# Performance work log

Measured on AMD Instinct MI355X. Metric: run time of the kernel, lower is better.

## Reference

```python
import jax, jax.numpy as jnp
import numpy as np

P, N, F, H, D_HID = 3, 4096, 1024, 8, 8
EMBED = H * D_HID  # 64
ATT, C = 128, 16


def setup_inputs() -> dict:
    key = jax.random.key(0)
    ks = jax.random.split(key, 12)
    return {
        "inputs": jax.random.normal(ks[0], (P, N, F), jnp.float32),
        # bias_mat plays the role of an additive adjacency mask; random floats are fine for math checking
        "bias_mat": jax.random.normal(ks[1], (P, N, N), jnp.float32),
        "W": jax.random.normal(ks[2], (P, H, F, D_HID), jnp.float32) * 0.05,
        "a1_w": jax.random.normal(ks[3], (P, H, D_HID), jnp.float32) * 0.1,
        "a1_b": jax.random.normal(ks[4], (P, H), jnp.float32) * 0.1,
        "a2_w": jax.random.normal(ks[5], (P, H, D_HID), jnp.float32) * 0.1,
        "a2_b": jax.random.normal(ks[6], (P, H), jnp.float32) * 0.1,
        "h_bias": jnp.zeros((P, H, D_HID), jnp.float32),
        "Ws": jax.random.normal(ks[7], (EMBED, ATT), jnp.float32) * 0.1,
        "bs": jax.random.normal(ks[8], (ATT,), jnp.float32) * 0.1,
        "u": jax.random.normal(ks[9], (ATT,), jnp.float32) * 0.1,
        "Wc": jax.random.normal(ks[10], (EMBED, C), jnp.float32) * 0.05,
        "bc": jnp.zeros((C,), jnp.float32),
    }


def reference(inputs, bias_mat, W, a1_w, a1_b, a2_w, a2_b, h_bias, Ws, bs, u, Wc, bc):
    # inputs: [P,N,F], bias_mat: [P,N,N]
    embeds = []
    for p in range(inputs.shape[0]):  # small fixed loop over meta-paths
        seq = inputs[p]                                            # [N,F]
        fts = jnp.einsum('nf,hfd->hnd', seq, W[p])                 # shared projection, all heads
        f1 = jnp.einsum('hnd,hd->hn', fts, a1_w[p]) + a1_b[p][:, None]
        f2 = jnp.einsum('hnd,hd->hn', fts, a2_w[p]) + a2_b[p][:, None]
        logits = f1[:, :, None] + f2[:, None, :]                   # [H,N,N] additive attention
        coefs = jax.nn.softmax(jax.nn.leaky_relu(logits) + bias_mat[p][None], axis=-1)
        vals = jnp.einsum('hnm,hmd->hnd', coefs, fts) + h_bias[p][:, None, :]
        h = jax.nn.elu(vals)                                       # activation per head
        embeds.append(jnp.transpose(h, (1, 0, 2)).reshape(h.shape[1], -1))  # concat heads -> [N,H*d]
    multi = jnp.stack(embeds, axis=1)                              # [N,P,EMBED]
    # semantic (meta-path) attention
    v = jnp.tanh(multi @ Ws + bs)                                  # [N,P,ATT]
    alphas = jax.nn.softmax(v @ u, axis=-1)                        # [N,P]
    final = jnp.sum(multi * alphas[:, :, None], axis=1)            # [N,EMBED]
    # single final classifier head (mean over 1 head == identity)
    logits_out = final @ Wc + bc                                   # [N,C]
    return logits_out, final, alphas
```

## Files before the change

kernel.cpp:

```cpp
#include <hip/hip_runtime.h>

#define LOG2E 1.44269504088896f

typedef _Float16 f16;
typedef _Float16 f16x8 __attribute__((ext_vector_type(8)));
typedef float f32x4 __attribute__((ext_vector_type(4)));

#define NP 3
#define NN 4096
#define FF 1024
#define HH 8
#define DD 8
#define HD 64

#define OFF_F1S   0
#define OFF_F2S   393216
#define OFF_F2MAX 589824
#define OFF_FTST  590080
#define OFF_MULTI 2162944

#define OUT_FINAL 65536
#define OUT_ALPHA 327680

__global__ __launch_bounds__(256) void kA(const float* __restrict__ inp,
                                          const float* __restrict__ W,
                                          const float* __restrict__ a1w,
                                          const float* __restrict__ a1b,
                                          const float* __restrict__ a2w,
                                          const float* __restrict__ a2b,
                                          char* __restrict__ ws) {
    __shared__ float At[32 * 36];
    __shared__ float Bt[32 * 64];
    __shared__ float ftile[32 * 68];
    const int tid = threadIdx.x;
    const int p = blockIdx.y;
    const int n0 = blockIdx.x * 32;

    const int tr = tid >> 4, tc = tid & 15;
    const int r0 = tr * 2, c0 = tc * 4;
    const int sr = tid >> 3, sak = (tid & 7) * 4;
    const int bc = tid & 63, bkq = tid >> 6;
    const int hB = bc >> 3, dB = bc & 7;

    float acc[2][4] = {};

    for (int kb = 0; kb < 32; ++kb) {
        const float* asrc = inp + ((size_t)p * NN + n0 + sr) * FF + kb * 32 + sak;
        float4 av = *(const float4*)asrc;
        At[(sak + 0) * 36 + sr] = av.x;
        At[(sak + 1) * 36 + sr] = av.y;
        At[(sak + 2) * 36 + sr] = av.z;
        At[(sak + 3) * 36 + sr] = av.w;
        #pragma unroll
        for (int i = 0; i < 8; ++i) {
            int k = bkq * 8 + i;
            Bt[k * 64 + bc] = W[(((size_t)p * HH + hB) * FF + kb * 32 + k) * DD + dB];
        }
        __syncthreads();
        #pragma unroll
        for (int k = 0; k < 32; ++k) {
            float2 a2 = *(const float2*)&At[k * 36 + r0];
            float4 bv = *(const float4*)&Bt[k * 64 + c0];
            float bb4[4] = {bv.x, bv.y, bv.z, bv.w};
            #pragma unroll
            for (int j = 0; j < 4; ++j) {
                acc[0][j] += a2.x * bb4[j];
                acc[1][j] += a2.y * bb4[j];
            }
        }
        __syncthreads();
    }
    #pragma unroll
    for (int i = 0; i < 2; ++i) {
        float4 o;
        o.x = acc[i][0]; o.y = acc[i][1]; o.z = acc[i][2]; o.w = acc[i][3];
        *(float4*)&ftile[(r0 + i) * 68 + c0] = o;
    }
    __syncthreads();

    float* f1s = (float*)(ws + OFF_F1S);
    f16* f2s = (f16*)(ws + OFF_F2S);
    {
        int row = tid >> 3, h = tid & 7;
        const float* fb = &ftile[row * 68 + h * 8];
        float s1 = a1b[p * HH + h], s2 = a2b[p * HH + h];
        #pragma unroll
        for (int d = 0; d < 8; ++d) {
            float v = fb[d];
            s1 += v * a1w[((size_t)p * HH + h) * DD + d];
            s2 += v * a2w[((size_t)p * HH + h) * DD + d];
        }
        f1s[((size_t)p * HH + h) * NN + n0 + row] = s1 * LOG2E;
        f2s[((size_t)p * HH + h) * NN + n0 + row] = (f16)(s2 * LOG2E);
    }
    {
        f16* ftsT = (f16*)(ws + OFF_FTST);
        int cc2 = tid >> 2, rq = (tid & 3) * 8;
        union { f16 h[8]; uint4 u; } pk;
        #pragma unroll
        for (int i = 0; i < 8; ++i) pk.h[i] = (f16)ftile[(rq + i) * 68 + cc2];
        *(uint4*)(ftsT + ((size_t)p * HD + cc2) * NN + n0 + rq) = pk.u;
    }
}

__global__ __launch_bounds__(64) void kA2(char* __restrict__ ws) {
    const f16* f2s = (const f16*)(ws + OFF_F2S);
    float* fmax = (float*)(ws + OFF_F2MAX);
    int b = blockIdx.x;
    int lane = threadIdx.x;
    float v = -1e30f;
    for (int m = lane; m < NN; m += 64) v = fmaxf(v, (float)f2s[(size_t)b * NN + m]);
    #pragma unroll
    for (int off = 32; off >= 1; off >>= 1) v = fmaxf(v, __shfl_xor(v, off, 64));
    if (lane == 0) fmax[b] = v;
}

__global__ __launch_bounds__(256, 3) void kB(const float* __restrict__ bias,
                                             const float* __restrict__ h_bias,
                                             char* __restrict__ ws) {
    __shared__ __align__(16) char smem[42768];
    f16* ftsL = (f16*)smem;
    float* f2L = (float*)(smem + 34320);

    const int tid = threadIdx.x;
    const int lane = tid & 63, wv = tid >> 6;
    const int c = lane & 15, kg = lane >> 4;
    const int p = blockIdx.y;
    const int n0 = blockIdx.x * 16;
    const int n = n0 + c;

    const float* f1s = (const float*)(ws + OFF_F1S);
    const f16* f2s = (const f16*)(ws + OFF_F2S);
    const float* fmax = (const float*)(ws + OFF_F2MAX);
    const f16* ftsG = (const f16*)(ws + OFF_FTST);
    float* multi = (float*)(ws + OFF_MULTI);

    float A1[8], B1[8];
    #pragma unroll
    for (int h = 0; h < 8; ++h) {
        float f1v = f1s[((size_t)p * 8 + h) * NN + n];
        float fm = fmax[p * 8 + h];
        float x = f1v + fm;
        float lr = fmaxf(x, 0.01f * x);
        float ub = lr + 8.0f * LOG2E;
        A1[h] = f1v - ub;
        B1[h] = fmaf(0.01f, f1v, -ub);
    }

    for (int i = tid; i < 264; i += 256) ftsL[64 * 264 + i] = (f16)1.0f;

    const int sg = tid >> 3, se = tid & 7;
    const int srow = sg & 7, sq = sg >> 3;
    const int f2r = tid >> 5, f2c = (tid & 31) * 8;

    const f16* ftsP = ftsG + (size_t)p * HD * NN + sq * 64 + se * 8;
    const f16* f2P = f2s + (size_t)p * 8 * NN + (size_t)f2r * NN + f2c;
    f16* ldst = ftsL + srow * 264 + sq * 64 + se * 8;

    const int rowsel = (c < 8) ? c * 264 : 64 * 264;
    const int hstep = (c < 8) ? 8 * 264 : 0;

    const float* bb_base = bias + ((size_t)p * NN + n) * NN + wv * 64 + kg * 8;

    f32x4 acc[8] = {};

    uint4 r0, r1, r2, r3, r4, r5, r6, r7, rv;

#define ISSUE(ch) do { \
        const f16* gs_ = ftsP + (ch) * 256; \
        r0 = *(const uint4*)(gs_ + (size_t)(srow +  0) * NN); \
        r1 = *(const uint4*)(gs_ + (size_t)(srow +  8) * NN); \
        r2 = *(const uint4*)(gs_ + (size_t)(srow + 16) * NN); \
        r3 = *(const uint4*)(gs_ + (size_t)(srow + 24) * NN); \
        r4 = *(const uint4*)(gs_ + (size_t)(srow + 32) * NN); \
        r5 = *(const uint4*)(gs_ + (size_t)(srow + 40) * NN); \
        r6 = *(const uint4*)(gs_ + (size_t)(srow + 48) * NN); \
        r7 = *(const uint4*)(gs_ + (size_t)(srow + 56) * NN); \
        rv = *(const uint4*)(f2P + (ch) * 256); \
    } while (0)

#define COMMIT() do { \
        *(uint4*)(ldst + 0 * 8 * 264) = r0; \
        *(uint4*)(ldst + 1 * 8 * 264) = r1; \
        *(uint4*)(ldst + 2 * 8 * 264) = r2; \
        *(uint4*)(ldst + 3 * 8 * 264) = r3; \
        *(uint4*)(ldst + 4 * 8 * 264) = r4; \
        *(uint4*)(ldst + 5 * 8 * 264) = r5; \
        *(uint4*)(ldst + 6 * 8 * 264) = r6; \
        *(uint4*)(ldst + 7 * 8 * 264) = r7; \
        union { uint4 u; f16 h[8]; } t16_; \
        t16_.u = rv; \
        float4 lo_, hi_; \
        lo_.x = (float)t16_.h[0]; lo_.y = (float)t16_.h[1]; \
        lo_.z = (float)t16_.h[2]; lo_.w = (float)t16_.h[3]; \
        hi_.x = (float)t16_.h[4]; hi_.y = (float)t16_.h[5]; \
        hi_.z = (float)t16_.h[6]; hi_.w = (float)t16_.h[7]; \
        *(float4*)(f2L + f2r * 264 + f2c) = lo_; \
        *(float4*)(f2L + f2r * 264 + f2c + 4) = hi_; \
    } while (0)

    ISSUE(0);
    COMMIT();
    ISSUE(1);
    float4 uA0 = *(const float4*)(bb_base);
    float4 uA1 = *(const float4*)(bb_base + 4);
    float4 uB0 = *(const float4*)(bb_base + 32);
    float4 uB1 = *(const float4*)(bb_base + 36);
    __syncthreads();

    #pragma unroll 1
    for (int ch = 0; ch < 16; ++ch) {
        const int chn = (ch + 1 < 16) ? ch + 1 : 15;
        const float* bpn = bb_base + chn * 256;
        float4 nA0 = *(const float4*)(bpn);
        float4 nA1 = *(const float4*)(bpn + 4);
        float4 nB0 = *(const float4*)(bpn + 32);
        float4 nB1 = *(const float4*)(bpn + 36);

        #pragma unroll
        for (int s = 0; s < 2; ++s) {
            const int mloc = wv * 64 + s * 32 + kg * 8;
            float4 bv0 = s ? uB0 : uA0;
            float4 bv1 = s ? uB1 : uA1;
            float bbl[8] = {bv0.x * LOG2E, bv0.y * LOG2E, bv0.z * LOG2E, bv0.w * LOG2E,
                            bv1.x * LOG2E, bv1.y * LOG2E, bv1.z * LOG2E, bv1.w * LOG2E};
            #pragma unroll
            for (int h = 0; h < 8; ++h) {
                const float* f2p = f2L + h * 264 + mloc;
                float4 f2a = *(const float4*)f2p;
                float4 f2b = *(const float4*)(f2p + 4);
                float f2arr[8] = {f2a.x, f2a.y, f2a.z, f2a.w, f2b.x, f2b.y, f2b.z, f2b.w};
                f16x8 bf = *(const f16x8*)(ftsL + rowsel + h * hstep + mloc);
                union { f16x8 v; f16 e[8]; } af;
                #pragma unroll
                for (int j = 0; j < 8; ++j) {
                    float t1 = f2arr[j] + A1[h];
                    float t2 = fmaf(0.01f, f2arr[j], B1[h]);
                    af.e[j] = (f16)__builtin_amdgcn_exp2f(fmaxf(t1, t2) + bbl[j]);
                }
                acc[h] = __builtin_amdgcn_mfma_f32_16x16x32_f16(af.v, bf, acc[h], 0, 0, 0);
            }
        }
        __syncthreads();
        if (ch < 15) {
            COMMIT();
            if (ch < 14) ISSUE(ch + 2);
            __syncthreads();
        }
        uA0 = nA0; uA1 = nA1; uB0 = nB0; uB1 = nB1;
    }
#undef ISSUE
#undef COMMIT

    float* red = (float*)smem;
    #pragma unroll
    for (int h = 0; h < 8; ++h) {
        if (c <= 8) {
            #pragma unroll
            for (int r = 0; r < 4; ++r)
                red[((wv * 8 + h) * 16 + kg * 4 + r) * 9 + c] = acc[h][r];
        }
    }
    __syncthreads();
    #pragma unroll
    for (int rep = 0; rep < 4; ++rep) {
        int idx = tid + rep * 256;
        int R = idx >> 6, hd = idx & 63;
        int h = hd >> 3, d = hd & 7;
        float v = 0.f, l = 0.f;
        #pragma unroll
        for (int w = 0; w < 4; ++w) {
            v += red[((w * 8 + h) * 16 + R) * 9 + d];
            l += red[((w * 8 + h) * 16 + R) * 9 + 8];
        }
        float o = v / l + h_bias[(p * 8 + h) * 8 + d];
        o = o > 0.f ? o : (__builtin_amdgcn_exp2f(o * LOG2E) - 1.0f);
        multi[((size_t)(n0 + R) * NP + p) * HD + hd] = o;
    }
}

__global__ __launch_bounds__(256) void kC(const float* __restrict__ Ws,
                                          const float* __restrict__ bsv,
                                          const float* __restrict__ uv,
                                          const float* __restrict__ Wc,
                                          const float* __restrict__ bcv,
                                          char* __restrict__ ws,
                                          float* __restrict__ out) {
    __shared__ float WsL[64 * 128];
    __shared__ float mult[16 * 3 * 64];
    __shared__ float WcL[64 * 16];
    __shared__ float uL[128], bsL[128], bcL[16];
    __shared__ float vred[16 * 3 * 16];
    __shared__ float alphaL[16 * 3];
    __shared__ float fin[16 * 64];
    const int tid = threadIdx.x;
    const int n0 = blockIdx.x * 16;
    const float* multi = (const float*)(ws + OFF_MULTI);

    for (int i = tid; i < 64 * 128; i += 256) WsL[i] = Ws[i];
    for (int i = tid; i < 3072; i += 256) mult[i] = multi[(size_t)n0 * 192 + i];
    for (int i = tid; i < 1024; i += 256) WcL[i] = Wc[i];
    if (tid < 128) { uL[tid] = uv[tid]; bsL[tid] = bsv[tid]; }
    if (tid < 16) bcL[tid] = bcv[tid];
    __syncthreads();

    const int nl = tid >> 4, j = tid & 15;
    for (int p = 0; p < 3; ++p) {
        float va[8] = {};
        for (int e = 0; e < 64; ++e) {
            float me = mult[(nl * 3 + p) * 64 + e];
            #pragma unroll
            for (int i = 0; i < 8; ++i) va[i] += me * WsL[e * 128 + j + 16 * i];
        }
        float part = 0.f;
        #pragma unroll
        for (int i = 0; i < 8; ++i) part += tanhf(va[i] + bsL[j + 16 * i]) * uL[j + 16 * i];
        vred[(nl * 3 + p) * 16 + j] = part;
    }
    __syncthreads();
    if (tid < 16) {
        float sc[3];
        for (int p = 0; p < 3; ++p) {
            float s = 0.f;
            for (int jj = 0; jj < 16; ++jj) s += vred[(tid * 3 + p) * 16 + jj];
            sc[p] = s;
        }
        float mx = fmaxf(sc[0], fmaxf(sc[1], sc[2]));
        float e0 = __builtin_amdgcn_exp2f((sc[0] - mx) * LOG2E);
        float e1 = __builtin_amdgcn_exp2f((sc[1] - mx) * LOG2E);
        float e2 = __builtin_amdgcn_exp2f((sc[2] - mx) * LOG2E);
        float inv = 1.f / (e0 + e1 + e2);
        float a0 = e0 * inv, a1 = e1 * inv, a2 = e2 * inv;
        alphaL[tid * 3 + 0] = a0; alphaL[tid * 3 + 1] = a1; alphaL[tid * 3 + 2] = a2;
        out[OUT_ALPHA + (size_t)(n0 + tid) * 3 + 0] = a0;
        out[OUT_ALPHA + (size_t)(n0 + tid) * 3 + 1] = a1;
        out[OUT_ALPHA + (size_t)(n0 + tid) * 3 + 2] = a2;
    }
    __syncthreads();
    for (int idx = tid; idx < 1024; idx += 256) {
        int nn2 = idx >> 6, e = idx & 63;
        float f = 0.f;
        for (int p = 0; p < 3; ++p) f += mult[(nn2 * 3 + p) * 64 + e] * alphaL[nn2 * 3 + p];
        fin[nn2 * 64 + e] = f;
        out[OUT_FINAL + (size_t)(n0 + nn2) * 64 + e] = f;
    }
    __syncthreads();
    {
        int nn2 = tid >> 4, cc2 = tid & 15;
        float lg = bcL[cc2];
        for (int e = 0; e < 64; ++e) lg += fin[nn2 * 64 + e] * WcL[e * 16 + cc2];
        out[(size_t)(n0 + nn2) * 16 + cc2] = lg;
    }
}

extern "C" void kernel_launch(void* const* d_in, const int* in_sizes, int n_in,
                              void* d_out, int out_size, void* d_ws, size_t ws_size,
                              hipStream_t stream) {
    (void)in_sizes; (void)n_in; (void)out_size; (void)ws_size;
    const float* inp = (const float*)d_in[0];
    const float* bias = (const float*)d_in[1];
    const float* W = (const float*)d_in[2];
    const float* a1w = (const float*)d_in[3];
    const float* a1b = (const float*)d_in[4];
    const float* a2w = (const float*)d_in[5];
    const float* a2b = (const float*)d_in[6];
    const float* hb = (const float*)d_in[7];
    const float* Wsv = (const float*)d_in[8];
    const float* bsv = (const float*)d_in[9];
    const float* uv = (const float*)d_in[10];
    const float* Wcv = (const float*)d_in[11];
    const float* bcv = (const float*)d_in[12];
    char* ws = (char*)d_ws;
    float* out = (float*)d_out;

    hipLaunchKernelGGL(kA, dim3(128, 3), dim3(256), 0, stream, inp, W, a1w, a1b, a2w, a2b, ws);
    hipLaunchKernelGGL(kA2, dim3(24), dim3(64), 0, stream, ws);
    hipLaunchKernelGGL(kB, dim3(256, 3), dim3(256), 0, stream, bias, hb, ws);
    hipLaunchKernelGGL(kC, dim3(256), dim3(256), 0, stream, Wsv, bsv, uv, Wcv, bcv, ws, out);
}
```

Baseline: 425.8 us.

## Prefetch next projection tiles into registers and vectorize W loads in kA

Restructures the kA projection GEMM so global loads for tile kb+2 are issued into registers while tile kb is computed, then committed to shared memory after the compute. The W tile load changes from eight scalar strided loads per thread to two float4 loads of contiguous head rows. The A-tile shared padding changes from 36 to 34. This targets global load latency in the projection stage, which is likely a minor share next to the attention kernel, at the cost of extra registers.

Measured after the change: 413.7 us. 2.8% less time.

```diff
diff --git a/kernel.cpp b/kernel.cpp
--- a/kernel.cpp
+++ b/kernel.cpp
@@ -29,7 +29,7 @@
                                           const float* __restrict__ a2w,
                                           const float* __restrict__ a2b,
                                           char* __restrict__ ws) {
-    __shared__ float At[32 * 36];
+    __shared__ float At[32 * 34];
     __shared__ float Bt[32 * 64];
     __shared__ float ftile[32 * 68];
     const int tid = threadIdx.x;
@@ -39,27 +39,42 @@
     const int tr = tid >> 4, tc = tid & 15;
     const int r0 = tr * 2, c0 = tc * 4;
     const int sr = tid >> 3, sak = (tid & 7) * 4;
-    const int bc = tid & 63, bkq = tid >> 6;
-    const int hB = bc >> 3, dB = bc & 7;
+    const int bk = tid >> 3, bh = tid & 7;
+
+    const float* aP = inp + ((size_t)p * NN + n0 + sr) * FF + sak;
+    const float* bP = W + (((size_t)p * HH + bh) * FF + bk) * DD;
+    float* bDst = &Bt[bk * 64 + bh * 8];
+
+    float4 pa, pb0, pb1;
+
+#define KA_ISSUE(kb) do { \
+        pa = *(const float4*)(aP + (kb) * 32); \
+        const float* bp_ = bP + (size_t)(kb) * 32 * DD; \
+        pb0 = *(const float4*)(bp_); \
+        pb1 = *(const float4*)(bp_ + 4); \
+    } while (0)
+
+#define KA_COMMIT() do { \
+        At[(sak + 0) * 34 + sr] = pa.x; \
+        At[(sak + 1) * 34 + sr] = pa.y; \
+        At[(sak + 2) * 34 + sr] = pa.z; \
+        At[(sak + 3) * 34 + sr] = pa.w; \
+        *(float4*)(bDst) = pb0; \
+        *(float4*)(bDst + 4) = pb1; \
+    } while (0)
 
     float acc[2][4] = {};
 
+    KA_ISSUE(0);
+    KA_COMMIT();
+    KA_ISSUE(1);
+    __syncthreads();
+
+    #pragma unroll 1
     for (int kb = 0; kb < 32; ++kb) {
-        const float* asrc = inp + ((size_t)p * NN + n0 + sr) * FF + kb * 32 + sak;
-        float4 av = *(const float4*)asrc;
-        At[(sak + 0) * 36 + sr] = av.x;
-        At[(sak + 1) * 36 + sr] = av.y;
-        At[(sak + 2) * 36 + sr] = av.z;
-        At[(sak + 3) * 36 + sr] = av.w;
-        #pragma unroll
-        for (int i = 0; i < 8; ++i) {
-            int k = bkq * 8 + i;
-            Bt[k * 64 + bc] = W[(((size_t)p * HH + hB) * FF + kb * 32 + k) * DD + dB];
-        }
-        __syncthreads();
         #pragma unroll
         for (int k = 0; k < 32; ++k) {
-            float2 a2 = *(const float2*)&At[k * 36 + r0];
+            float2 a2 = *(const float2*)&At[k * 34 + r0];
             float4 bv = *(const float4*)&Bt[k * 64 + c0];
             float bb4[4] = {bv.x, bv.y, bv.z, bv.w};
             #pragma unroll
@@ -69,7 +84,15 @@
             }
         }
         __syncthreads();
-    }
+        if (kb < 31) {
+            KA_COMMIT();
+            if (kb < 30) KA_ISSUE(kb + 2);
+            __syncthreads();
+        }
+    }
+#undef KA_ISSUE
+#undef KA_COMMIT
+
     #pragma unroll
     for (int i = 0; i < 2; ++i) {
         float4 o;
```
